# Kernel tuning notes

Measured on AMD Instinct MI355X. Metric: run time of the kernel, lower is better.

## Reference

```python
import jax, jax.numpy as jnp
import numpy as np

NUM_HEADS = 8
DIM_HEAD = 64
SCALE = DIM_HEAD * NUM_HEADS  # q *= dim_head * num_heads, as in the source


def setup_inputs() -> dict:
    key = jax.random.key(0)
    k1, k2, k3, k4 = jax.random.split(key, 4)
    B, C, H, W = 8, 64, 32, 32
    x = jax.random.normal(k1, (B, C, H, W), dtype=jnp.float32)
    # 1x1 conv == matmul over channels; small init keeps post-scale logits sane
    w_qkv = jax.random.normal(k2, (3 * NUM_HEADS * DIM_HEAD, C), dtype=jnp.float32) * 0.02
    rel_h = jax.random.normal(k3, (2 * H - 1, DIM_HEAD), dtype=jnp.float32) * 0.02
    rel_w = jax.random.normal(k4, (2 * W - 1, DIM_HEAD), dtype=jnp.float32) * 0.02
    return {"x": x, "w_qkv": w_qkv, "rel_h": rel_h, "rel_w": rel_w}


def _rel_indices(H, W):
    # flattened 2D grid positions
    pos_y = np.repeat(np.arange(H), W)  # [HW]
    pos_x = np.tile(np.arange(W), H)    # [HW]
    rel_y = pos_y[None, :] - pos_y[:, None] + (H - 1)  # [HW, HW] in [0, 2H-2]
    rel_x = pos_x[None, :] - pos_x[:, None] + (W - 1)  # [HW, HW] in [0, 2W-2]
    return jnp.asarray(rel_y), jnp.asarray(rel_x)


def reference(x, w_qkv, rel_h, rel_w):
    B, C, H, W = x.shape
    n = H * W
    # 1x1 conv (bias=False) -> per-pixel matmul
    xf = x.reshape(B, C, n)                              # b c n
    qkv = jnp.einsum('oc,bcn->bon', w_qkv, xf)           # b (3 h d) n
    q, k, v = jnp.split(qkv, 3, axis=1)
    def to_heads(t):  # b (h d) n -> b h n d
        return t.reshape(B, NUM_HEADS, DIM_HEAD, n).transpose(0, 1, 3, 2)
    q, k, v = to_heads(q), to_heads(k), to_heads(v)
    q = q * SCALE  # scale applied before QK^T AND before pos bias (in-place in torch)

    sim = jnp.einsum('bhid,bhjd->bhij', q, k)            # [B, h, n, n]

    # relative position bias: q_i . rel_h[dy] + q_i . rel_w[dx]
    logits_h = jnp.einsum('bhid,rd->bhir', q, rel_h)     # [B, h, n, 2H-1]
    logits_w = jnp.einsum('bhid,rd->bhir', q, rel_w)     # [B, h, n, 2W-1]
    rel_y, rel_x = _rel_indices(H, W)                    # [n, n] each
    i_idx = jnp.arange(n)[:, None]                       # [n, 1]
    bias = logits_h[:, :, i_idx, rel_y] + logits_w[:, :, i_idx, rel_x]  # [B,h,n,n]

    attn = jax.nn.softmax(sim + bias, axis=-1)
    out = jnp.einsum('bhij,bhjd->bhid', attn, v)         # [B, h, n, d]
    out = out.transpose(0, 1, 3, 2).reshape(B, NUM_HEADS * DIM_HEAD, H, W)
    return out
```

## Files before the change

kernel.cpp:

```cpp
#include <hip/hip_runtime.h>
#include <hip/hip_bf16.h>
#include <hip/hip_fp16.h>

typedef _Float16 h8 __attribute__((ext_vector_type(8)));
typedef unsigned short us8 __attribute__((ext_vector_type(8)));
typedef float f4 __attribute__((ext_vector_type(4)));

#define NH 8
#define DH 64
#define NPIX 1024
#define CIN 64
#define NBH 64
#define QSCALE (512.0f * 1.44269504f)
#define LOSCALE 2048.0f
#define INV_LOSCALE (1.0f / 2048.0f)
#define DTHR 12.0f

__device__ __forceinline__ void gload_lds16(const void* g, void* lds) {
  __builtin_amdgcn_global_load_lds(
      (const __attribute__((address_space(1))) void*)g,
      (__attribute__((address_space(3))) void*)lds, 16, 0, 0);
}

template <int CTRL>
__device__ __forceinline__ float dpp_ror(float x) {
  return __int_as_float(__builtin_amdgcn_update_dpp(
      0, __float_as_int(x), CTRL, 0xF, 0xF, true));
}

__device__ __forceinline__ float fexp2(float x) {
#if __has_builtin(__builtin_amdgcn_exp2f)
  return __builtin_amdgcn_exp2f(x);
#else
  return exp2f(x);
#endif
}

__global__ __launch_bounds__(256) void qkv_mfma(
    const float* __restrict__ x, const float* __restrict__ wqkv,
    _Float16* __restrict__ Qh, _Float16* __restrict__ Ql,
    _Float16* __restrict__ Kh, _Float16* __restrict__ Kl,
    _Float16* __restrict__ Vv) {
  __shared__ __align__(16) char QS[49152];
  char* Wh = QS;
  char* Wl = QS + 16384;
  char* Xh = QS + 32768;
  char* Xl = QS + 40960;

  const int tid = threadIdx.x;
  const int lane = tid & 63;
  const int w = tid >> 6;
  const int c = lane & 15;
  const int g = lane >> 4;
  const int o0 = blockIdx.x * 128;
  const int p0 = blockIdx.y * 64;
  const int b = blockIdx.z;

  #pragma unroll
  for (int it = 0; it < 4; ++it) {
    int task = tid + it * 256;
    int oct = task & 7, o = task >> 3;
    const f4* wr = (const f4*)(wqkv + (size_t)(o0 + o) * CIN + oct * 8);
    f4 wa = wr[0], wb = wr[1];
    h8 hi, lo;
    #pragma unroll
    for (int e = 0; e < 8; ++e) {
      float v = e < 4 ? wa[e] : wb[e - 4];
      _Float16 h = (_Float16)v;
      hi[e] = h;
      lo[e] = (_Float16)((v - (float)h) * LOSCALE);
    }
    int byo = o * 128 + ((oct ^ (o & 7)) << 4);
    *(h8*)(Wh + byo) = hi;
    *(h8*)(Wl + byo) = lo;
  }
  #pragma unroll
  for (int it = 0; it < 16; ++it) {
    int idx = tid + it * 256;
    int p = idx & 63, cc = idx >> 6;
    float v = x[((size_t)b * CIN + cc) * NPIX + p0 + p];
    _Float16 h = (_Float16)v;
    _Float16 l = (_Float16)((v - (float)h) * LOSCALE);
    int byo = p * 128 + (((cc >> 3) ^ (p & 7)) << 4) + (cc & 7) * 2;
    *(_Float16*)(Xh + byo) = h;
    *(_Float16*)(Xl + byo) = l;
  }
  __syncthreads();

  f4 zf = {0.f, 0.f, 0.f, 0.f};
  f4 acc[2][4], cor[2][4];
  #pragma unroll
  for (int oi = 0; oi < 2; ++oi)
    #pragma unroll
    for (int pi = 0; pi < 4; ++pi) { acc[oi][pi] = zf; cor[oi][pi] = zf; }

  const int ob = w * 32;
  #pragma unroll
  for (int kh = 0; kh < 2; ++kh) {
    h8 ah[2], al[2], bh[4], bl[4];
    #pragma unroll
    for (int oi = 0; oi < 2; ++oi) {
      int orow = ob + ((c >> 2) << 3) + (c & 3) + oi * 4;
      int ch = (((kh * 4 + g) ^ (orow & 7)) << 4);
      ah[oi] = *(const h8*)(Wh + orow * 128 + ch);
      al[oi] = *(const h8*)(Wl + orow * 128 + ch);
    }
    #pragma unroll
    for (int pi = 0; pi < 4; ++pi) {
      int prow = pi * 16 + c;
      int ch = (((kh * 4 + g) ^ (prow & 7)) << 4);
      bh[pi] = *(const h8*)(Xh + prow * 128 + ch);
      bl[pi] = *(const h8*)(Xl + prow * 128 + ch);
    }
    __builtin_amdgcn_s_setprio(1);
    #pragma unroll
    for (int oi = 0; oi < 2; ++oi)
      #pragma unroll
      for (int pi = 0; pi < 4; ++pi) {
        acc[oi][pi] = __builtin_amdgcn_mfma_f32_16x16x32_f16(ah[oi], bh[pi], acc[oi][pi], 0, 0, 0);
        cor[oi][pi] = __builtin_amdgcn_mfma_f32_16x16x32_f16(ah[oi], bl[pi], cor[oi][pi], 0, 0, 0);
        cor[oi][pi] = __builtin_amdgcn_mfma_f32_16x16x32_f16(al[oi], bh[pi], cor[oi][pi], 0, 0, 0);
      }
    __builtin_amdgcn_s_setprio(0);
  }

  const int part = o0 >> 9;
  const float scl = part == 0 ? QSCALE : 1.0f;
  _Float16* dsth = part == 0 ? Qh : (part == 1 ? Kh : Vv);
  _Float16* dstl = part == 0 ? Ql : (part == 1 ? Kl : nullptr);
  #pragma unroll
  for (int pi = 0; pi < 4; ++pi) {
    int obase = o0 + ob + 8 * g;
    int h = (obase >> 6) & 7;
    int d = obase & 63;
    int p_abs = p0 + pi * 16 + c;
    size_t off = (((size_t)(b * NH + h)) * NPIX + p_abs) * DH + d;
    h8 hv, lv;
    #pragma unroll
    for (int oi = 0; oi < 2; ++oi)
      #pragma unroll
      for (int reg = 0; reg < 4; ++reg) {
        float v = (acc[oi][pi][reg] + cor[oi][pi][reg] * INV_LOSCALE) * scl;
        _Float16 hh = (_Float16)v;
        hv[oi * 4 + reg] = hh;
        lv[oi * 4 + reg] = (_Float16)((v - (float)hh) * LOSCALE);
      }
    *(h8*)(dsth + off) = hv;
    if (dstl) *(h8*)(dstl + off) = lv;
  }
}

__global__ __launch_bounds__(256, 2) void attn_mfma(
    const _Float16* __restrict__ Qh, const _Float16* __restrict__ Ql,
    const _Float16* __restrict__ Kh, const _Float16* __restrict__ Kl,
    const _Float16* __restrict__ V,
    const float* __restrict__ rel_h, const float* __restrict__ rel_w,
    float* __restrict__ out) {
  __shared__ __align__(16) char SMem[81920];
  char* SMp = SMem + 49152;
  _Float16* LWT16 = (_Float16*)SMp;
  _Float16* LH16 = (_Float16*)(SMem + 65536);
  float* OT = (float*)SMem;

  const int tid = threadIdx.x;
  const int lane = tid & 63;
  const int w = tid >> 6;
  const int wu = __builtin_amdgcn_readfirstlane(w);
  const int c = lane & 15;
  const int g = lane >> 4;
  const int bx = blockIdx.x;
  const int bh = ((bx & 7) << 3) | ((bx >> 3) & 7);
  const int i0 = (bx >> 6) << 7;

  const _Float16* Qhg = Qh + (size_t)bh * NPIX * DH;
  const _Float16* Qlg = Ql + (size_t)bh * NPIX * DH;
  const _Float16* Khg = Kh + (size_t)bh * NPIX * DH;
  const _Float16* Klg = Kl + (size_t)bh * NPIX * DH;
  const _Float16* Vg  = V  + (size_t)bh * NPIX * DH;

  const h8* Qr0h = (const h8*)(Qhg + (size_t)(i0 + w * 32 + c) * DH);
  const h8* Qr0l = (const h8*)(Qlg + (size_t)(i0 + w * 32 + c) * DH);
  const h8* Qr1h = (const h8*)(Qhg + (size_t)(i0 + w * 32 + 16 + c) * DH);
  const h8* Qr1l = (const h8*)(Qlg + (size_t)(i0 + w * 32 + 16 + c) * DH);
  h8 q0h[2] = {Qr0h[g], Qr0h[4 + g]};
  h8 q0l[2] = {Qr0l[g], Qr0l[4 + g]};
  h8 q1h[2] = {Qr1h[g], Qr1h[4 + g]};
  h8 q1l[2] = {Qr1l[g], Qr1l[4 + g]};

  const int s0i = wu * 128 + lane;
  const int s1i = s0i + 64;
  const int ko0 = (s0i >> 3) * 128 + (((s0i & 7) ^ ((s0i >> 3) & 7)) << 4);
  const int ko1 = (s1i >> 3) * 128 + (((s1i & 7) ^ ((s1i >> 3) & 7)) << 4);

  #pragma unroll
  for (int it = 0; it < 2; ++it) {
    int task = tid + it * 256;
    int oct = task & 7, s = task >> 3;
    int ss = s < 63 ? s : 62;
    const float* sh = rel_h + (size_t)ss * DH + oct * 8;
    const float* sw = rel_w + (size_t)ss * DH + oct * 8;
    h8 hh, ww;
    #pragma unroll
    for (int e = 0; e < 8; ++e) {
      hh[e] = (_Float16)sh[e];
      ww[e] = (_Float16)sw[e];
    }
    int byo = s * 128 + ((oct ^ (s & 7)) << 4);
    *(h8*)(SMem + byo) = hh;
    *(h8*)(SMem + 32768 + byo) = ww;
  }
  __syncthreads();

  f4 zf = {0.f, 0.f, 0.f, 0.f};
  #pragma unroll
  for (int rs = 0; rs < 2; ++rs) {
    f4 lhC[4], lwC[4], lhCc[4], lwCc[4];
    #pragma unroll
    for (int cg = 0; cg < 4; ++cg) { lhC[cg] = zf; lwC[cg] = zf; lhCc[cg] = zf; lwCc[cg] = zf; }
    #pragma unroll
    for (int kh = 0; kh < 2; ++kh) {
      h8 a  = rs ? q1h[kh] : q0h[kh];
      h8 al = rs ? q1l[kh] : q0l[kh];
      #pragma unroll
      for (int cg = 0; cg < 4; ++cg) {
        int s = cg * 16 + c;
        int chb = s * 128 + (((kh * 4 + g) ^ (s & 7)) << 4);
        h8 rb = *(const h8*)(SMem + chb);
        h8 wb = *(const h8*)(SMem + 32768 + chb);
        lhC[cg]  = __builtin_amdgcn_mfma_f32_16x16x32_f16(a,  rb, lhC[cg], 0, 0, 0);
        lhCc[cg] = __builtin_amdgcn_mfma_f32_16x16x32_f16(al, rb, lhCc[cg], 0, 0, 0);
        lwC[cg]  = __builtin_amdgcn_mfma_f32_16x16x32_f16(a,  wb, lwC[cg], 0, 0, 0);
        lwCc[cg] = __builtin_amdgcn_mfma_f32_16x16x32_f16(al, wb, lwCc[cg], 0, 0, 0);
      }
    }
    #pragma unroll
    for (int cg = 0; cg < 4; ++cg)
      #pragma unroll
      for (int reg = 0; reg < 4; ++reg) {
        int r = w * 32 + rs * 16 + 4 * g + reg;
        int col = cg * 16 + c;
        LH16[r * 64 + (col ^ (((r >> 2) & 3) << 4))] =
            (_Float16)(lhC[cg][reg] + lhCc[cg][reg] * INV_LOSCALE);
        LWT16[r * 64 + col] =
            (_Float16)(lwC[cg][reg] + lwCc[cg][reg] * INV_LOSCALE);
      }
  }
  __syncthreads();

  float lw0[4][2], lw1[4][2];
  #pragma unroll
  for (int reg = 0; reg < 4; ++reg) {
    int xi0 = 4 * g + reg;
    int r0 = w * 32 + xi0;
    #pragma unroll
    for (int par = 0; par < 2; ++par) {
      lw0[reg][par] = (float)LWT16[r0 * 64 + 31 + par * 16 + c - xi0];
      lw1[reg][par] = (float)LWT16[(r0 + 16) * 64 + 31 + par * 16 + c - (xi0 + 16)];
    }
  }

  {
    gload_lds16((const char*)Khg + ko0, SMem + wu * 2048);
    gload_lds16((const char*)Khg + ko1, SMem + wu * 2048 + 1024);
    gload_lds16((const char*)Klg + ko0, SMem + 16384 + wu * 2048);
    gload_lds16((const char*)Klg + ko1, SMem + 16384 + wu * 2048 + 1024);
    int jp = tid & 31, dd = tid >> 5;
    const h8* vr = (const h8*)(Vg + (size_t)(2 * jp) * DH);
    h8 v0 = vr[dd], v1 = vr[8 + dd];
    us8 u0 = *(const us8*)&v0, u1 = *(const us8*)&v1;
    #pragma unroll
    for (int e = 0; e < 8; ++e) {
      int d = dd * 8 + e;
      unsigned int val = (unsigned int)u0[e] | ((unsigned int)u1[e] << 16);
      *(unsigned int*)(SMem + 32768 + d * 128 + (((jp >> 2) ^ (d & 7)) << 4) + (jp & 3) * 4) = val;
    }
  }
  __syncthreads();

  const int yi = (i0 >> 5) + w;
  float m0[4], lp0[4], m1[4], lp1[4];
  f4 o0_[4], o1_[4];
  #pragma unroll
  for (int reg = 0; reg < 4; ++reg) { m0[reg] = -1e30f; lp0[reg] = 0.f; m1[reg] = -1e30f; lp1[reg] = 0.f; }
  #pragma unroll
  for (int cg = 0; cg < 4; ++cg) { o0_[cg] = zf; o1_[cg] = zf; }

  int cur = 0;
  #pragma unroll 1
  for (int t = 0; t < 16; ++t) {
    char* Kc  = SMem + cur * 8192;
    char* KLc = SMem + 16384 + cur * 8192;
    char* Vc  = SMem + 32768 + cur * 8192;
    const int nxt = cur ^ 1;
    const bool pre = t < 15;
    const int jp = tid & 31, dd = tid >> 5;
    h8 v0 = {}, v1 = {};
    if (pre) {
      const char* kg  = (const char*)Khg + (size_t)(t + 1) * 8192;
      const char* klg = (const char*)Klg + (size_t)(t + 1) * 8192;
      char* Kn  = SMem + nxt * 8192;
      char* KLn = SMem + 16384 + nxt * 8192;
      gload_lds16(kg + ko0, Kn + wu * 2048);
      gload_lds16(kg + ko1, Kn + wu * 2048 + 1024);
      gload_lds16(klg + ko0, KLn + wu * 2048);
      gload_lds16(klg + ko1, KLn + wu * 2048 + 1024);
      const h8* vr = (const h8*)(Vg + (size_t)((t + 1) * 64 + 2 * jp) * DH);
      v0 = vr[dd];
      v1 = vr[8 + dd];
    }

    f4 s0_[4], sc0_[4], s1_[4], sc1_[4];
    #pragma unroll
    for (int cg = 0; cg < 4; ++cg) { s0_[cg] = zf; sc0_[cg] = zf; s1_[cg] = zf; sc1_[cg] = zf; }
    #pragma unroll
    for (int kh = 0; kh < 2; ++kh) {
      h8 a0 = q0h[kh], a0l = q0l[kh], a1 = q1h[kh], a1l = q1l[kh];
      #pragma unroll
      for (int cg = 0; cg < 4; ++cg) {
        int j = cg * 16 + c;
        int chb = j * 128 + (((kh * 4 + g) ^ (j & 7)) << 4);
        h8 kbh = *(const h8*)(Kc + chb);
        h8 kbl = *(const h8*)(KLc + chb);
        __builtin_amdgcn_s_setprio(1);
        s0_[cg]  = __builtin_amdgcn_mfma_f32_16x16x32_f16(a0,  kbh, s0_[cg], 0, 0, 0);
        sc0_[cg] = __builtin_amdgcn_mfma_f32_16x16x32_f16(a0l, kbh, sc0_[cg], 0, 0, 0);
        sc0_[cg] = __builtin_amdgcn_mfma_f32_16x16x32_f16(a0,  kbl, sc0_[cg], 0, 0, 0);
        s1_[cg]  = __builtin_amdgcn_mfma_f32_16x16x32_f16(a1,  kbh, s1_[cg], 0, 0, 0);
        sc1_[cg] = __builtin_amdgcn_mfma_f32_16x16x32_f16(a1l, kbh, sc1_[cg], 0, 0, 0);
        sc1_[cg] = __builtin_amdgcn_mfma_f32_16x16x32_f16(a1,  kbl, sc1_[cg], 0, 0, 0);
        __builtin_amdgcn_s_setprio(0);
      }
    }

    const int lhb = 31 + 2 * t - yi;
    auto finish = [&](f4* s_, f4* sc_, float (*lw)[2], float* m_s, float* lp,
                      f4* o_, int rs) {
      float lhv[4][2];
      #pragma unroll
      for (int reg = 0; reg < 4; ++reg) {
        int r = w * 32 + rs * 16 + 4 * g + reg;
        int msk = ((r >> 2) & 3) << 4;
        lhv[reg][0] = (float)LH16[r * 64 + (lhb ^ msk)];
        lhv[reg][1] = (float)LH16[r * 64 + ((lhb + 1) ^ msk)];
      }
      #pragma unroll
      for (int cg = 0; cg < 4; ++cg)
        #pragma unroll
        for (int reg = 0; reg < 4; ++reg)
          s_[cg][reg] += sc_[cg][reg] * INV_LOSCALE + lw[reg][cg & 1] + lhv[reg][cg >> 1];
      float tm[4];
      int skip = 1;
      #pragma unroll
      for (int reg = 0; reg < 4; ++reg) {
        float v = fmaxf(fmaxf(s_[0][reg], s_[1][reg]), fmaxf(s_[2][reg], s_[3][reg]));
        v = fmaxf(v, dpp_ror<0x121>(v));
        v = fmaxf(v, dpp_ror<0x122>(v));
        v = fmaxf(v, dpp_ror<0x124>(v));
        v = fmaxf(v, dpp_ror<0x128>(v));
        tm[reg] = v;
        skip &= (v <= m_s[reg] + DTHR) ? 1 : 0;
      }
      float pvv[4][4];
      if (__all(skip)) {
        #pragma unroll
        for (int reg = 0; reg < 4; ++reg) {
          float sum = 0.f;
          #pragma unroll
          for (int cg = 0; cg < 4; ++cg) {
            float p = fexp2(s_[cg][reg] - m_s[reg]);
            pvv[cg][reg] = p;
            sum += p;
          }
          lp[reg] += sum;
        }
      } else {
        #pragma unroll
        for (int reg = 0; reg < 4; ++reg) {
          float mn = fmaxf(m_s[reg], tm[reg]);
          float corr = fexp2(m_s[reg] - mn);
          m_s[reg] = mn;
          float sum = 0.f;
          #pragma unroll
          for (int cg = 0; cg < 4; ++cg) {
            float p = fexp2(s_[cg][reg] - mn);
            pvv[cg][reg] = p;
            sum += p;
          }
          lp[reg] = lp[reg] * corr + sum;
          #pragma unroll
          for (int cg = 0; cg < 4; ++cg) o_[cg][reg] *= corr;
        }
      }
      #pragma unroll
      for (int reg = 0; reg < 4; ++reg) {
        int r2 = rs * 16 + 4 * g + reg;
        #pragma unroll
        for (int cg = 0; cg < 4; ++cg) {
          int j = cg * 16 + c;
          *(_Float16*)(SMp + w * 4096 + r2 * 128 + (((j >> 3) ^ (r2 & 7)) << 4) + (j & 7) * 2)
              = (_Float16)pvv[cg][reg];
        }
      }
    };

    finish(s0_, sc0_, lw0, m0, lp0, o0_, 0);
    __builtin_amdgcn_wave_barrier();

    h8 vbr[2][4];
    #pragma unroll
    for (int kh = 0; kh < 2; ++kh) {
      int oc = kh * 4 + g;
      h8 pa0 = *(const h8*)(SMp + w * 4096 + c * 128 + ((oc ^ (c & 7)) << 4));
      __builtin_amdgcn_s_setprio(1);
      #pragma unroll
      for (int cgd = 0; cgd < 4; ++cgd) {
        int d = cgd * 16 + c;
        vbr[kh][cgd] = *(const h8*)(Vc + d * 128 + ((oc ^ (d & 7)) << 4));
        o0_[cgd] = __builtin_amdgcn_mfma_f32_16x16x32_f16(pa0, vbr[kh][cgd], o0_[cgd], 0, 0, 0);
      }
      __builtin_amdgcn_s_setprio(0);
    }
    finish(s1_, sc1_, lw1, m1, lp1, o1_, 1);
    __builtin_amdgcn_wave_barrier();

    #pragma unroll
    for (int kh = 0; kh < 2; ++kh) {
      int oc = kh * 4 + g;
      h8 pa1 = *(const h8*)(SMp + w * 4096 + (16 + c) * 128 + ((oc ^ (c & 7)) << 4));
      __builtin_amdgcn_s_setprio(1);
      #pragma unroll
      for (int cgd = 0; cgd < 4; ++cgd)
        o1_[cgd] = __builtin_amdgcn_mfma_f32_16x16x32_f16(pa1, vbr[kh][cgd], o1_[cgd], 0, 0, 0);
      __builtin_amdgcn_s_setprio(0);
    }

    if (pre) {
      us8 u0 = *(const us8*)&v0, u1 = *(const us8*)&v1;
      char* Vn = SMem + 32768 + nxt * 8192;
      #pragma unroll
      for (int e = 0; e < 8; ++e) {
        int d = dd * 8 + e;
        unsigned int val = (unsigned int)u0[e] | ((unsigned int)u1[e] << 16);
        *(unsigned int*)(Vn + d * 128 + (((jp >> 2) ^ (d & 7)) << 4) + (jp & 3) * 4) = val;
      }
    }
    __syncthreads();
    cur = nxt;
  }

  float r0v[4], r1v[4];
  #pragma unroll
  for (int reg = 0; reg < 4; ++reg) {
    float a = lp0[reg];
    a += dpp_ror<0x121>(a);
    a += dpp_ror<0x122>(a);
    a += dpp_ror<0x124>(a);
    a += dpp_ror<0x128>(a);
    r0v[reg] = __builtin_amdgcn_rcpf(a);
    float b = lp1[reg];
    b += dpp_ror<0x121>(b);
    b += dpp_ror<0x122>(b);
    b += dpp_ror<0x124>(b);
    b += dpp_ror<0x128>(b);
    r1v[reg] = __builtin_amdgcn_rcpf(b);
  }
  #pragma unroll
  for (int cgd = 0; cgd < 4; ++cgd)
    #pragma unroll
    for (int reg = 0; reg < 4; ++reg) {
      int d = cgd * 16 + c;
      int sw = (d & 7) << 3;
      int r0 = w * 32 + 4 * g + reg;
      OT[d * 128 + (r0 ^ sw)] = o0_[cgd][reg] * r0v[reg];
      OT[d * 128 + ((r0 + 16) ^ sw)] = o1_[cgd][reg] * r1v[reg];
    }
  __syncthreads();
  #pragma unroll
  for (int it = 0; it < 8; ++it) {
    int task = tid + it * 256;
    int rq = task & 31, d = task >> 5;
    f4 vv = *(const f4*)&OT[d * 128 + ((rq * 4) ^ ((d & 7) << 3))];
    *(f4*)(out + (((size_t)bh * 64 + d) << 10) + i0 + rq * 4) = vv;
  }
}

extern "C" void kernel_launch(void* const* d_in, const int* in_sizes, int n_in,
                              void* d_out, int out_size, void* d_ws, size_t ws_size,
                              hipStream_t stream) {
  const float* x  = (const float*)d_in[0];
  const float* wq = (const float*)d_in[1];
  const float* rh = (const float*)d_in[2];
  const float* rw = (const float*)d_in[3];
  float* out = (float*)d_out;

  const size_t sz = (size_t)NBH * NPIX * DH;
  _Float16* Qh = (_Float16*)d_ws;
  _Float16* Ql = Qh + sz;
  _Float16* Kh = Ql + sz;
  _Float16* Kl = Kh + sz;
  _Float16* V  = Kl + sz;

  qkv_mfma<<<dim3(12, 16, 8), 256, 0, stream>>>(x, wq, Qh, Ql, Kh, Kl, V);
  attn_mfma<<<dim3(512), 256, 0, stream>>>(Qh, Ql, Kh, Kl, V, rh, rw, out);
}
```

Measured before the change: 88.60 us.

## Transpose attention MFMA operands so softmax row reductions become lane-local

Swaps the A/B operands of the QK^T and PV MFMAs so each lane holds a full query row's scores in its registers. The row max and sum then need only two cross-lane shuffles instead of per-register DPP rotate chains, and the online-softmax state shrinks to one scalar per row. The change also precomputes a compacted per-row rel_h bias table, packs P into LDS with cvt_pkrtz, and cuts LDS use to 64KB, which may help occupancy. The new layouts and swizzles add risk of indexing mistakes, and the round-toward-zero conversion of P changes rounding slightly.

Result: faster. 79.86 us (-9.9%).

```diff
diff --git a/kernel.cpp b/kernel.cpp
--- a/kernel.cpp
+++ b/kernel.cpp
@@ -3,6 +3,7 @@
 #include <hip/hip_fp16.h>
 
 typedef _Float16 h8 __attribute__((ext_vector_type(8)));
+typedef _Float16 h2 __attribute__((ext_vector_type(2)));
 typedef unsigned short us8 __attribute__((ext_vector_type(8)));
 typedef float f4 __attribute__((ext_vector_type(4)));
 
@@ -22,18 +23,26 @@
       (__attribute__((address_space(3))) void*)lds, 16, 0, 0);
 }
 
-template <int CTRL>
-__device__ __forceinline__ float dpp_ror(float x) {
-  return __int_as_float(__builtin_amdgcn_update_dpp(
-      0, __float_as_int(x), CTRL, 0xF, 0xF, true));
-}
-
 __device__ __forceinline__ float fexp2(float x) {
 #if __has_builtin(__builtin_amdgcn_exp2f)
   return __builtin_amdgcn_exp2f(x);
 #else
   return exp2f(x);
 #endif
+}
+
+__device__ __forceinline__ unsigned pk16(float a, float b) {
+  auto r = __builtin_amdgcn_cvt_pkrtz(a, b);
+  union { decltype(r) h; unsigned u; } x;
+  x.h = r;
+  return x.u;
+}
+
+__device__ __forceinline__ f4 max4(f4 a, f4 b) {
+  f4 r;
+  r[0] = fmaxf(a[0], b[0]); r[1] = fmaxf(a[1], b[1]);
+  r[2] = fmaxf(a[2], b[2]); r[3] = fmaxf(a[3], b[3]);
+  return r;
 }
 
 __global__ __launch_bounds__(256) void qkv_mfma(
@@ -156,10 +165,10 @@
     const _Float16* __restrict__ V,
     const float* __restrict__ rel_h, const float* __restrict__ rel_w,
     float* __restrict__ out) {
-  __shared__ __align__(16) char SMem[81920];
-  char* SMp = SMem + 49152;
-  _Float16* LWT16 = (_Float16*)SMp;
-  _Float16* LH16 = (_Float16*)(SMem + 65536);
+  __shared__ __align__(16) char SMem[65536];
+  char* SP = SMem + 49152;
+  _Float16* LHc = (_Float16*)(SMem + 57344);
+  _Float16* LWT = (_Float16*)(SMem + 32768);
   float* OT = (float*)SMem;
 
   const int tid = threadIdx.x;
@@ -171,6 +180,7 @@
   const int bx = blockIdx.x;
   const int bh = ((bx & 7) << 3) | ((bx >> 3) & 7);
   const int i0 = (bx >> 6) << 7;
+  const int swz = (c & 7) << 4;
 
   const _Float16* Qhg = Qh + (size_t)bh * NPIX * DH;
   const _Float16* Qlg = Ql + (size_t)bh * NPIX * DH;
@@ -207,57 +217,57 @@
     }
     int byo = s * 128 + ((oct ^ (s & 7)) << 4);
     *(h8*)(SMem + byo) = hh;
-    *(h8*)(SMem + 32768 + byo) = ww;
-  }
-  __syncthreads();
-
+    *(h8*)(SMem + 16384 + byo) = ww;
+  }
+  __syncthreads();
+
+  const int yi = (i0 + w * 32) >> 5;
   f4 zf = {0.f, 0.f, 0.f, 0.f};
   #pragma unroll
   for (int rs = 0; rs < 2; ++rs) {
-    f4 lhC[4], lwC[4], lhCc[4], lwCc[4];
-    #pragma unroll
-    for (int cg = 0; cg < 4; ++cg) { lhC[cg] = zf; lwC[cg] = zf; lhCc[cg] = zf; lwCc[cg] = zf; }
+    f4 lhD[4], lwD[4], lhDc[4], lwDc[4];
+    #pragma unroll
+    for (int st = 0; st < 4; ++st) { lhD[st] = zf; lwD[st] = zf; lhDc[st] = zf; lwDc[st] = zf; }
     #pragma unroll
     for (int kh = 0; kh < 2; ++kh) {
-      h8 a  = rs ? q1h[kh] : q0h[kh];
-      h8 al = rs ? q1l[kh] : q0l[kh];
-      #pragma unroll
-      for (int cg = 0; cg < 4; ++cg) {
-        int s = cg * 16 + c;
-        int chb = s * 128 + (((kh * 4 + g) ^ (s & 7)) << 4);
-        h8 rb = *(const h8*)(SMem + chb);
-        h8 wb = *(const h8*)(SMem + 32768 + chb);
-        lhC[cg]  = __builtin_amdgcn_mfma_f32_16x16x32_f16(a,  rb, lhC[cg], 0, 0, 0);
-        lhCc[cg] = __builtin_amdgcn_mfma_f32_16x16x32_f16(al, rb, lhCc[cg], 0, 0, 0);
-        lwC[cg]  = __builtin_amdgcn_mfma_f32_16x16x32_f16(a,  wb, lwC[cg], 0, 0, 0);
-        lwCc[cg] = __builtin_amdgcn_mfma_f32_16x16x32_f16(al, wb, lwCc[cg], 0, 0, 0);
-      }
-    }
-    #pragma unroll
-    for (int cg = 0; cg < 4; ++cg)
+      h8 bq = rs ? q1h[kh] : q0h[kh];
+      h8 bl = rs ? q1l[kh] : q0l[kh];
+      #pragma unroll
+      for (int st = 0; st < 4; ++st) {
+        int srow = st * 16 + c;
+        int chb = srow * 128 + (((kh * 4 + g) ^ (srow & 7)) << 4);
+        h8 ra = *(const h8*)(SMem + chb);
+        h8 wa = *(const h8*)(SMem + 16384 + chb);
+        lhD[st]  = __builtin_amdgcn_mfma_f32_16x16x32_f16(ra, bq, lhD[st], 0, 0, 0);
+        lhDc[st] = __builtin_amdgcn_mfma_f32_16x16x32_f16(ra, bl, lhDc[st], 0, 0, 0);
+        lwD[st]  = __builtin_amdgcn_mfma_f32_16x16x32_f16(wa, bq, lwD[st], 0, 0, 0);
+        lwDc[st] = __builtin_amdgcn_mfma_f32_16x16x32_f16(wa, bl, lwDc[st], 0, 0, 0);
+      }
+    }
+    int lrow = w * 32 + rs * 16 + c;
+    #pragma unroll
+    for (int st = 0; st < 4; ++st)
       #pragma unroll
       for (int reg = 0; reg < 4; ++reg) {
-        int r = w * 32 + rs * 16 + 4 * g + reg;
-        int col = cg * 16 + c;
-        LH16[r * 64 + (col ^ (((r >> 2) & 3) << 4))] =
-            (_Float16)(lhC[cg][reg] + lhCc[cg][reg] * INV_LOSCALE);
-        LWT16[r * 64 + col] =
-            (_Float16)(lwC[cg][reg] + lwCc[cg][reg] * INV_LOSCALE);
-      }
-  }
-  __syncthreads();
-
-  float lw0[4][2], lw1[4][2];
-  #pragma unroll
-  for (int reg = 0; reg < 4; ++reg) {
-    int xi0 = 4 * g + reg;
-    int r0 = w * 32 + xi0;
-    #pragma unroll
-    for (int par = 0; par < 2; ++par) {
-      lw0[reg][par] = (float)LWT16[r0 * 64 + 31 + par * 16 + c - xi0];
-      lw1[reg][par] = (float)LWT16[(r0 + 16) * 64 + 31 + par * 16 + c - (xi0 + 16)];
-    }
-  }
+        int s = st * 16 + 4 * g + reg;
+        float lhv = lhD[st][reg] + lhDc[st][reg] * INV_LOSCALE;
+        float lwv = lwD[st][reg] + lwDc[st][reg] * INV_LOSCALE;
+        int k = s - 31 + yi;
+        if (k >= 0 && k < 32) LHc[lrow * 32 + k] = (_Float16)lhv;
+        LWT[lrow * 64 + s] = (_Float16)lwv;
+      }
+  }
+  __syncthreads();
+
+  h8 lwp0, lwp1;
+  #pragma unroll
+  for (int jbp = 0; jbp < 2; ++jbp)
+    #pragma unroll
+    for (int reg = 0; reg < 4; ++reg) {
+      lwp0[jbp * 4 + reg] = LWT[(w * 32 + c) * 64 + 31 + jbp * 16 + 4 * g + reg - c];
+      lwp1[jbp * 4 + reg] = LWT[(w * 32 + 16 + c) * 64 + 31 + jbp * 16 + 4 * g + reg - 16 - c];
+    }
+  __syncthreads();
 
   {
     gload_lds16((const char*)Khg + ko0, SMem + wu * 2048);
@@ -277,13 +287,10 @@
   }
   __syncthreads();
 
-  const int yi = (i0 >> 5) + w;
-  float m0[4], lp0[4], m1[4], lp1[4];
+  float m0 = -1e30f, m1 = -1e30f, lp0 = 0.f, lp1 = 0.f;
   f4 o0_[4], o1_[4];
   #pragma unroll
-  for (int reg = 0; reg < 4; ++reg) { m0[reg] = -1e30f; lp0[reg] = 0.f; m1[reg] = -1e30f; lp1[reg] = 0.f; }
-  #pragma unroll
-  for (int cg = 0; cg < 4; ++cg) { o0_[cg] = zf; o1_[cg] = zf; }
+  for (int dt = 0; dt < 4; ++dt) { o0_[dt] = zf; o1_[dt] = zf; }
 
   int cur = 0;
   #pragma unroll 1
@@ -298,139 +305,111 @@
     if (pre) {
       const char* kg  = (const char*)Khg + (size_t)(t + 1) * 8192;
       const char* klg = (const char*)Klg + (size_t)(t + 1) * 8192;
-      char* Kn  = SMem + nxt * 8192;
-      char* KLn = SMem + 16384 + nxt * 8192;
-      gload_lds16(kg + ko0, Kn + wu * 2048);
-      gload_lds16(kg + ko1, Kn + wu * 2048 + 1024);
-      gload_lds16(klg + ko0, KLn + wu * 2048);
-      gload_lds16(klg + ko1, KLn + wu * 2048 + 1024);
+      gload_lds16(kg + ko0, SMem + nxt * 8192 + wu * 2048);
+      gload_lds16(kg + ko1, SMem + nxt * 8192 + wu * 2048 + 1024);
+      gload_lds16(klg + ko0, SMem + 16384 + nxt * 8192 + wu * 2048);
+      gload_lds16(klg + ko1, SMem + 16384 + nxt * 8192 + wu * 2048 + 1024);
       const h8* vr = (const h8*)(Vg + (size_t)((t + 1) * 64 + 2 * jp) * DH);
       v0 = vr[dd];
       v1 = vr[8 + dd];
     }
 
-    f4 s0_[4], sc0_[4], s1_[4], sc1_[4];
-    #pragma unroll
-    for (int cg = 0; cg < 4; ++cg) { s0_[cg] = zf; sc0_[cg] = zf; s1_[cg] = zf; sc1_[cg] = zf; }
+    f4 s0[4], c0[4], s1[4], c1[4];
+    #pragma unroll
+    for (int jb = 0; jb < 4; ++jb) { s0[jb] = zf; c0[jb] = zf; s1[jb] = zf; c1[jb] = zf; }
     #pragma unroll
     for (int kh = 0; kh < 2; ++kh) {
-      h8 a0 = q0h[kh], a0l = q0l[kh], a1 = q1h[kh], a1l = q1l[kh];
-      #pragma unroll
-      for (int cg = 0; cg < 4; ++cg) {
-        int j = cg * 16 + c;
-        int chb = j * 128 + (((kh * 4 + g) ^ (j & 7)) << 4);
-        h8 kbh = *(const h8*)(Kc + chb);
-        h8 kbl = *(const h8*)(KLc + chb);
+      h8 b0h = q0h[kh], b0l = q0l[kh], b1h = q1h[kh], b1l = q1l[kh];
+      #pragma unroll
+      for (int jb = 0; jb < 4; ++jb) {
+        int jrow = jb * 16 + c;
+        int chb = jrow * 128 + (((kh * 4 + g) ^ (c & 7)) << 4);
+        h8 ah = *(const h8*)(Kc + chb);
+        h8 al = *(const h8*)(KLc + chb);
         __builtin_amdgcn_s_setprio(1);
-        s0_[cg]  = __builtin_amdgcn_mfma_f32_16x16x32_f16(a0,  kbh, s0_[cg], 0, 0, 0);
-        sc0_[cg] = __builtin_amdgcn_mfma_f32_16x16x32_f16(a0l, kbh, sc0_[cg], 0, 0, 0);
-        sc0_[cg] = __builtin_amdgcn_mfma_f32_16x16x32_f16(a0,  kbl, sc0_[cg], 0, 0, 0);
-        s1_[cg]  = __builtin_amdgcn_mfma_f32_16x16x32_f16(a1,  kbh, s1_[cg], 0, 0, 0);
-        sc1_[cg] = __builtin_amdgcn_mfma_f32_16x16x32_f16(a1l, kbh, sc1_[cg], 0, 0, 0);
-        sc1_[cg] = __builtin_amdgcn_mfma_f32_16x16x32_f16(a1,  kbl, sc1_[cg], 0, 0, 0);
+        s0[jb] = __builtin_amdgcn_mfma_f32_16x16x32_f16(ah, b0h, s0[jb], 0, 0, 0);
+        c0[jb] = __builtin_amdgcn_mfma_f32_16x16x32_f16(al, b0h, c0[jb], 0, 0, 0);
+        c0[jb] = __builtin_amdgcn_mfma_f32_16x16x32_f16(ah, b0l, c0[jb], 0, 0, 0);
+        s1[jb] = __builtin_amdgcn_mfma_f32_16x16x32_f16(ah, b1h, s1[jb], 0, 0, 0);
+        c1[jb] = __builtin_amdgcn_mfma_f32_16x16x32_f16(al, b1h, c1[jb], 0, 0, 0);
+        c1[jb] = __builtin_amdgcn_mfma_f32_16x16x32_f16(ah, b1l, c1[jb], 0, 0, 0);
         __builtin_amdgcn_s_setprio(0);
       }
     }
 
-    const int lhb = 31 + 2 * t - yi;
-    auto finish = [&](f4* s_, f4* sc_, float (*lw)[2], float* m_s, float* lp,
+    auto finish = [&](f4* s_, f4* c_, const h8& lwp, float& m_s, float& lp,
                       f4* o_, int rs) {
-      float lhv[4][2];
-      #pragma unroll
-      for (int reg = 0; reg < 4; ++reg) {
-        int r = w * 32 + rs * 16 + 4 * g + reg;
-        int msk = ((r >> 2) & 3) << 4;
-        lhv[reg][0] = (float)LH16[r * 64 + (lhb ^ msk)];
-        lhv[reg][1] = (float)LH16[r * 64 + ((lhb + 1) ^ msk)];
-      }
-      #pragma unroll
-      for (int cg = 0; cg < 4; ++cg)
+      h2 lhu = *(const h2*)(LHc + (w * 32 + rs * 16 + c) * 32 + 2 * t);
+      float lh01[2] = {(float)lhu[0], (float)lhu[1]};
+      #pragma unroll
+      for (int jb = 0; jb < 4; ++jb)
         #pragma unroll
         for (int reg = 0; reg < 4; ++reg)
-          s_[cg][reg] += sc_[cg][reg] * INV_LOSCALE + lw[reg][cg & 1] + lhv[reg][cg >> 1];
-      float tm[4];
-      int skip = 1;
-      #pragma unroll
-      for (int reg = 0; reg < 4; ++reg) {
-        float v = fmaxf(fmaxf(s_[0][reg], s_[1][reg]), fmaxf(s_[2][reg], s_[3][reg]));
-        v = fmaxf(v, dpp_ror<0x121>(v));
-        v = fmaxf(v, dpp_ror<0x122>(v));
-        v = fmaxf(v, dpp_ror<0x124>(v));
-        v = fmaxf(v, dpp_ror<0x128>(v));
-        tm[reg] = v;
-        skip &= (v <= m_s[reg] + DTHR) ? 1 : 0;
-      }
-      float pvv[4][4];
-      if (__all(skip)) {
+          s_[jb][reg] += c_[jb][reg] * INV_LOSCALE +
+                         (float)lwp[(jb & 1) * 4 + reg] + lh01[jb >> 1];
+      f4 ab = max4(s_[0], s_[1]);
+      f4 cd = max4(s_[2], s_[3]);
+      f4 ef = max4(ab, cd);
+      float mx = fmaxf(fmaxf(ef[0], ef[1]), fmaxf(ef[2], ef[3]));
+      mx = fmaxf(mx, __shfl_xor(mx, 16, 64));
+      mx = fmaxf(mx, __shfl_xor(mx, 32, 64));
+      bool sk = mx <= m_s + DTHR;
+      if (!__all(sk)) {
+        float mn = fmaxf(m_s, mx);
+        float corr = fexp2(m_s - mn);
+        m_s = mn;
+        lp *= corr;
+        #pragma unroll
+        for (int dt = 0; dt < 4; ++dt)
+          #pragma unroll
+          for (int reg = 0; reg < 4; ++reg)
+            o_[dt][reg] *= corr;
+      }
+      float sum = 0.f;
+      char* pbse = SP + w * 2048 + c * 128;
+      #pragma unroll
+      for (int jb = 0; jb < 4; ++jb) {
+        f4 p;
         #pragma unroll
         for (int reg = 0; reg < 4; ++reg) {
-          float sum = 0.f;
-          #pragma unroll
-          for (int cg = 0; cg < 4; ++cg) {
-            float p = fexp2(s_[cg][reg] - m_s[reg]);
-            pvv[cg][reg] = p;
-            sum += p;
-          }
-          lp[reg] += sum;
+          p[reg] = fexp2(s_[jb][reg] - m_s);
+          sum += p[reg];
         }
-      } else {
-        #pragma unroll
-        for (int reg = 0; reg < 4; ++reg) {
-          float mn = fmaxf(m_s[reg], tm[reg]);
-          float corr = fexp2(m_s[reg] - mn);
-          m_s[reg] = mn;
-          float sum = 0.f;
-          #pragma unroll
-          for (int cg = 0; cg < 4; ++cg) {
-            float p = fexp2(s_[cg][reg] - mn);
-            pvv[cg][reg] = p;
-            sum += p;
-          }
-          lp[reg] = lp[reg] * corr + sum;
-          #pragma unroll
-          for (int cg = 0; cg < 4; ++cg) o_[cg][reg] *= corr;
-        }
-      }
-      #pragma unroll
-      for (int reg = 0; reg < 4; ++reg) {
-        int r2 = rs * 16 + 4 * g + reg;
-        #pragma unroll
-        for (int cg = 0; cg < 4; ++cg) {
-          int j = cg * 16 + c;
-          *(_Float16*)(SMp + w * 4096 + r2 * 128 + (((j >> 3) ^ (r2 & 7)) << 4) + (j & 7) * 2)
-              = (_Float16)pvv[cg][reg];
-        }
-      }
+        *(unsigned*)(pbse + ((jb * 32 + 8 * g) ^ swz)) = pk16(p[0], p[1]);
+        *(unsigned*)(pbse + ((jb * 32 + 8 * g + 4) ^ swz)) = pk16(p[2], p[3]);
+      }
+      lp += sum;
     };
 
-    finish(s0_, sc0_, lw0, m0, lp0, o0_, 0);
+    finish(s0, c0, lwp0, m0, lp0, o0_, 0);
     __builtin_amdgcn_wave_barrier();
 
     h8 vbr[2][4];
     #pragma unroll
     for (int kh = 0; kh < 2; ++kh) {
-      int oc = kh * 4 + g;
-      h8 pa0 = *(const h8*)(SMp + w * 4096 + c * 128 + ((oc ^ (c & 7)) << 4));
+      int och = ((kh * 4 + g) ^ (c & 7)) << 4;
+      h8 pb = *(const h8*)(SP + w * 2048 + c * 128 + och);
       __builtin_amdgcn_s_setprio(1);
       #pragma unroll
-      for (int cgd = 0; cgd < 4; ++cgd) {
-        int d = cgd * 16 + c;
-        vbr[kh][cgd] = *(const h8*)(Vc + d * 128 + ((oc ^ (d & 7)) << 4));
-        o0_[cgd] = __builtin_amdgcn_mfma_f32_16x16x32_f16(pa0, vbr[kh][cgd], o0_[cgd], 0, 0, 0);
+      for (int dt = 0; dt < 4; ++dt) {
+        vbr[kh][dt] = *(const h8*)(Vc + (dt * 16 + c) * 128 + och);
+        o0_[dt] = __builtin_amdgcn_mfma_f32_16x16x32_f16(vbr[kh][dt], pb, o0_[dt], 0, 0, 0);
       }
       __builtin_amdgcn_s_setprio(0);
     }
-    finish(s1_, sc1_, lw1, m1, lp1, o1_, 1);
     __builtin_amdgcn_wave_barrier();
 
+    finish(s1, c1, lwp1, m1, lp1, o1_, 1);
+    __builtin_amdgcn_wave_barrier();
+
     #pragma unroll
     for (int kh = 0; kh < 2; ++kh) {
-      int oc = kh * 4 + g;
-      h8 pa1 = *(const h8*)(SMp + w * 4096 + (16 + c) * 128 + ((oc ^ (c & 7)) << 4));
+      int och = ((kh * 4 + g) ^ (c & 7)) << 4;
+      h8 pb = *(const h8*)(SP + w * 2048 + c * 128 + och);
       __builtin_amdgcn_s_setprio(1);
       #pragma unroll
-      for (int cgd = 0; cgd < 4; ++cgd)
-        o1_[cgd] = __builtin_amdgcn_mfma_f32_16x16x32_f16(pa1, vbr[kh][cgd], o1_[cgd], 0, 0, 0);
+      for (int dt = 0; dt < 4; ++dt)
+        o1_[dt] = __builtin_amdgcn_mfma_f32_16x16x32_f16(vbr[kh][dt], pb, o1_[dt], 0, 0, 0);
       __builtin_amdgcn_s_setprio(0);
     }
 
@@ -448,31 +427,23 @@
     cur = nxt;
   }
 
-  float r0v[4], r1v[4];
-  #pragma unroll
-  for (int reg = 0; reg < 4; ++reg) {
-    float a = lp0[reg];
-    a += dpp_ror<0x121>(a);
-    a += dpp_ror<0x122>(a);
-    a += dpp_ror<0x124>(a);
-    a += dpp_ror<0x128>(a);
-    r0v[reg] = __builtin_amdgcn_rcpf(a);
-    float b = lp1[reg];
-    b += dpp_ror<0x121>(b);
-    b += dpp_ror<0x122>(b);
-    b += dpp_ror<0x124>(b);
-    b += dpp_ror<0x128>(b);
-    r1v[reg] = __builtin_amdgcn_rcpf(b);
-  }
-  #pragma unroll
-  for (int cgd = 0; cgd < 4; ++cgd)
+  float a0 = lp0;
+  a0 += __shfl_xor(a0, 16, 64);
+  a0 += __shfl_xor(a0, 32, 64);
+  float r0 = __builtin_amdgcn_rcpf(a0);
+  float a1 = lp1;
+  a1 += __shfl_xor(a1, 16, 64);
+  a1 += __shfl_xor(a1, 32, 64);
+  float r1 = __builtin_amdgcn_rcpf(a1);
+  #pragma unroll
+  for (int dt = 0; dt < 4; ++dt)
     #pragma unroll
     for (int reg = 0; reg < 4; ++reg) {
-      int d = cgd * 16 + c;
+      int d = dt * 16 + 4 * g + reg;
       int sw = (d & 7) << 3;
-      int r0 = w * 32 + 4 * g + reg;
-      OT[d * 128 + (r0 ^ sw)] = o0_[cgd][reg] * r0v[reg];
-      OT[d * 128 + ((r0 + 16) ^ sw)] = o1_[cgd][reg] * r1v[reg];
+      int il0 = w * 32 + c;
+      OT[d * 128 + (il0 ^ sw)] = o0_[dt][reg] * r0;
+      OT[d * 128 + ((il0 + 16) ^ sw)] = o1_[dt][reg] * r1;
     }
   __syncthreads();
   #pragma unroll
```
